# Kernel tuning notes

Measured on AMD Instinct MI355X. Metric: run time of the kernel, lower is better.

## Reference

```python
import jax, jax.numpy as jnp
import numpy as np

NUM_CLUSTERS = 64
DIM = 256
EPS = 1e-12  # torch F.normalize eps


def setup_inputs() -> dict:
    key = jax.random.key(0)
    k1, k2, k3, k4 = jax.random.split(key, 4)
    x = jax.random.normal(k1, (128, DIM, 32, 32), dtype=jnp.float32)
    # nn.Conv2d(256, K, 1) params: weight (K, C, 1, 1) -> store as (K, C); bias (K,)
    fan_in = DIM
    bound = 1.0 / np.sqrt(fan_in)
    conv_w = jax.random.uniform(k2, (NUM_CLUSTERS, DIM), jnp.float32, -bound, bound)
    conv_b = jax.random.uniform(k3, (NUM_CLUSTERS,), jnp.float32, -bound, bound)
    centroids = jax.random.uniform(k4, (NUM_CLUSTERS, DIM), jnp.float32)  # torch.rand
    return {"x": x, "conv_w": conv_w, "conv_b": conv_b, "centroids": centroids}


def _l2norm(v, axis):
    n = jnp.sqrt(jnp.sum(v * v, axis=axis, keepdims=True))
    return v / jnp.maximum(n, EPS)


def reference(x, conv_w, conv_b, centroids):
    N, C, H, W = x.shape
    K = conv_w.shape[0]
    # L2-normalize over channel dim
    x = _l2norm(x, axis=1)                      # (N, C, H, W)
    xf = x.reshape(N, C, H * W)                 # (N, C, P)
    # 1x1 conv == per-pixel linear over channels
    logits = jnp.einsum('ncp,kc->nkp', xf, conv_w) + conv_b[None, :, None]
    a = jax.nn.softmax(logits, axis=1)          # (N, K, P) softmax over clusters
    # VLAD via matmul decomposition: sum_p a[n,k,p]*(x[n,:,p] - c[k,:])
    agg = jnp.einsum('nkp,ncp->nkc', a, xf)     # (N, K, C)
    asum = jnp.sum(a, axis=-1)                  # (N, K)
    vlad = agg - asum[:, :, None] * centroids[None, :, :]
    vlad = _l2norm(vlad, axis=2)                # intra-normalization
    vlad = vlad.reshape(N, K * C)
    return _l2norm(vlad, axis=1)
```

## Files before the change

### kernel.cpp

```cpp
#include <hip/hip_runtime.h>
#include <math.h>


#define EPSF 1e-12f

typedef __attribute__((ext_vector_type(8))) __bf16 bf16x8;
typedef __attribute__((ext_vector_type(4))) float f32x4;
typedef __attribute__((ext_vector_type(4))) unsigned int u32x4;

#define MFMA(a, b, c) __builtin_amdgcn_mfma_f32_16x16x32_bf16((a), (b), (c), 0, 0, 0)

__device__ __forceinline__ bf16x8 as_bf(u32x4 v) { return __builtin_bit_cast(bf16x8, v); }

__device__ __forceinline__ unsigned packsplit(float x) {
    const unsigned u  = __float_as_uint(x);
    const unsigned hi = u & 0xFFFF0000u;
    const float lof   = x - __uint_as_float(hi);
    return hi | (__float_as_uint(lof) >> 16);
}

struct u32pair { unsigned h, l; };

__device__ __forceinline__ u32pair splitpair(float f0, float f1) {
    const unsigned u0 = __float_as_uint(f0), u1 = __float_as_uint(f1);
    u32pair r;
    r.h = __builtin_amdgcn_perm(u1, u0, 0x07060302u);
    const float l0 = f0 - __uint_as_float(u0 & 0xFFFF0000u);
    const float l1 = f1 - __uint_as_float(u1 & 0xFFFF0000u);
    r.l = __builtin_amdgcn_perm(__float_as_uint(l1), __float_as_uint(l0), 0x07060302u);
    return r;
}

__device__ __forceinline__ void unpack2q(const u32x4 q0, const u32x4 q1,
                                         u32x4& hi, u32x4& lo) {
    hi[0] = __builtin_amdgcn_perm(q0[1], q0[0], 0x07060302u);
    lo[0] = __builtin_amdgcn_perm(q0[1], q0[0], 0x05040100u);
    hi[1] = __builtin_amdgcn_perm(q0[3], q0[2], 0x07060302u);
    lo[1] = __builtin_amdgcn_perm(q0[3], q0[2], 0x05040100u);
    hi[2] = __builtin_amdgcn_perm(q1[1], q1[0], 0x07060302u);
    lo[2] = __builtin_amdgcn_perm(q1[1], q1[0], 0x05040100u);
    hi[3] = __builtin_amdgcn_perm(q1[3], q1[2], 0x07060302u);
    lo[3] = __builtin_amdgcn_perm(q1[3], q1[2], 0x05040100u);
}

__device__ __forceinline__ void split8v(const float* xv, u32x4& hi, u32x4& lo) {
    #pragma unroll
    for (int w2 = 0; w2 < 4; ++w2) {
        const u32pair r = splitpair(xv[2*w2], xv[2*w2+1]);
        hi[w2] = r.h;
        lo[w2] = r.l;
    }
}

__global__ void split_w_kernel(const float* __restrict__ wmat,
                               unsigned* __restrict__ whiG,
                               unsigned* __restrict__ wloG) {
    const int idx = blockIdx.x * 256 + threadIdx.x;
    const int mt = idx >> 9, s = (idx >> 6) & 7, l = idx & 63;
    const int k = mt * 16 + (l & 15);
    const int cb = s * 32 + 8 * (l >> 4);
    const float* wr = wmat + k * 256 + cb;
    const float4 f0 = *(const float4*)wr;
    const float4 f1 = *(const float4*)(wr + 4);
    const float xv[8] = {f0.x, f0.y, f0.z, f0.w, f1.x, f1.y, f1.z, f1.w};
    u32x4 hi, lo; split8v(xv, hi, lo);
    *(u32x4*)(whiG + idx * 4) = hi;
    *(u32x4*)(wloG + idx * 4) = lo;
}

__global__ __launch_bounds__(256, 4) void netvlad_mfma(
    const float* __restrict__ x,
    const unsigned* __restrict__ whiG, const unsigned* __restrict__ wloG,
    const float* __restrict__ bias, float* __restrict__ out,
    float* __restrict__ asum_g) {

    __shared__ __align__(16) unsigned smem[8704];
    __shared__ __align__(16) float rn_lds[128];
    unsigned* const abuf = smem;
    unsigned* const p2hi = smem;
    unsigned* const p2lo = smem + 4352;

    const int t = threadIdx.x;
    const int w = t >> 6, l = t & 63;
    const int l15 = l & 15, lg4 = l >> 4;
    const int n = blockIdx.x & 127, e = blockIdx.x >> 7;
    const size_t ximg = (size_t)n * 256 * 1024;
    const int p0 = e * 128;
    const int k0 = w * 16;
    const int cs = lg4 * 8;

    f32x4 acc1[4][2];
    #pragma unroll
    for (int i = 0; i < 4; ++i) {
        acc1[i][0] = f32x4{0.f, 0.f, 0.f, 0.f};
        acc1[i][1] = f32x4{0.f, 0.f, 0.f, 0.f};
    }
    float ssa[2] = {0.f, 0.f};

    #pragma unroll
    for (int s = 0; s < 8; ++s) {
        u32x4 wh[4], wl[4];
        #pragma unroll
        for (int mt = 0; mt < 4; ++mt) {
            const int fo = ((mt * 8 + s) * 64 + l) * 4;
            wh[mt] = *(const u32x4*)(whiG + fo);
            wl[mt] = *(const u32x4*)(wloG + fo);
        }
        #pragma unroll
        for (int ntl = 0; ntl < 2; ++ntl) {
            const float* bp = x + ximg + (size_t)(s * 32 + cs) * 1024
                              + p0 + (2 * w + ntl) * 16 + l15;
            float xv[8];
            #pragma unroll
            for (int j = 0; j < 8; ++j) xv[j] = bp[(size_t)j * 1024];
            #pragma unroll
            for (int j = 0; j < 8; ++j) ssa[ntl] = fmaf(xv[j], xv[j], ssa[ntl]);
            u32x4 bhi, blo; split8v(xv, bhi, blo);
            #pragma unroll
            for (int mt = 0; mt < 4; ++mt) {
                acc1[mt][ntl] = MFMA(as_bf(wh[mt]), as_bf(bhi), acc1[mt][ntl]);
                acc1[mt][ntl] = MFMA(as_bf(wh[mt]), as_bf(blo), acc1[mt][ntl]);
                acc1[mt][ntl] = MFMA(as_bf(wl[mt]), as_bf(bhi), acc1[mt][ntl]);
            }
        }
    }
    #pragma unroll
    for (int ntl = 0; ntl < 2; ++ntl) {
        ssa[ntl] += __shfl_xor(ssa[ntl], 16);
        ssa[ntl] += __shfl_xor(ssa[ntl], 32);
    }

    f32x4 biasv[4];
    #pragma unroll
    for (int mt = 0; mt < 4; ++mt)
        biasv[mt] = *(const f32x4*)(bias + mt * 16 + 4 * lg4);

    const int r2 = t >> 4;
    const int pq8 = (t & 15) * 8;
    const float* xg2 = x + ximg + (size_t)r2 * 1024 + p0 + pq8;
    unsigned* const w2hi = p2hi + r2 * 68 + (pq8 >> 1);
    unsigned* const w2lo = p2lo + r2 * 68 + (pq8 >> 1);
    float4 g2[4];
    #define P2_LOAD(s_) { _Pragma("unroll")                                   \
        for (int i = 0; i < 2; ++i) {                                         \
            g2[i*2]   = *(const float4*)(xg2 + (size_t)((s_)*32 + 16*i)*1024);    \
            g2[i*2+1] = *(const float4*)(xg2 + (size_t)((s_)*32 + 16*i)*1024 + 4);\
        } }
    #define P2_WRITE(b_) { _Pragma("unroll")                                  \
        for (int i = 0; i < 2; ++i) {                                         \
            u32x4 vh, vl;                                                     \
            const u32pair ra = splitpair(g2[i*2].x,   g2[i*2].y);             \
            const u32pair rb = splitpair(g2[i*2].z,   g2[i*2].w);             \
            const u32pair rc = splitpair(g2[i*2+1].x, g2[i*2+1].y);           \
            const u32pair rd = splitpair(g2[i*2+1].z, g2[i*2+1].w);           \
            vh[0] = ra.h; vl[0] = ra.l;                                       \
            vh[1] = rb.h; vl[1] = rb.l;                                       \
            vh[2] = rc.h; vl[2] = rc.l;                                       \
            vh[3] = rd.h; vl[3] = rd.l;                                       \
            *(u32x4*)(w2hi + (b_) * 2176 + i * 1088) = vh;                    \
            *(u32x4*)(w2lo + (b_) * 2176 + i * 1088) = vl; } }
    P2_LOAD(0);

    #pragma unroll
    for (int ntl = 0; ntl < 2; ++ntl) {
        const int p = (2 * w + ntl) * 16 + l15;
        const float rn = 1.f / fmaxf(sqrtf(ssa[ntl]), EPSF);
        if (lg4 == 0) rn_lds[p] = rn;
        float lgv[16];
        #pragma unroll
        for (int mt = 0; mt < 4; ++mt)
            #pragma unroll
            for (int r = 0; r < 4; ++r)
                lgv[mt * 4 + r] = fmaf(acc1[mt][ntl][r], rn, biasv[mt][r]);
        float mx = lgv[0];
        #pragma unroll
        for (int i = 1; i < 16; ++i) mx = fmaxf(mx, lgv[i]);
        mx = fmaxf(mx, __shfl_xor(mx, 16));
        mx = fmaxf(mx, __shfl_xor(mx, 32));
        float den = 0.f;
        #pragma unroll
        for (int i = 0; i < 16; ++i) { lgv[i] = __expf(lgv[i] - mx); den += lgv[i]; }
        den += __shfl_xor(den, 16);
        den += __shfl_xor(den, 32);
        const float inv = 1.f / den;
        #pragma unroll
        for (int mt = 0; mt < 4; ++mt)
            #pragma unroll
            for (int r = 0; r < 4; ++r)
                abuf[(mt * 16 + 4 * lg4 + r) * 132 + p] =
                    packsplit(lgv[mt * 4 + r] * inv);
    }
    __syncthreads();

    u32x4 aphi[4], aplo[4];
    f32x4 asum_acc = f32x4{0.f, 0.f, 0.f, 0.f};
    const u32x4 ONES = {0x3F803F80u, 0x3F803F80u, 0x3F803F80u, 0x3F803F80u};
    #pragma unroll
    for (int ks = 0; ks < 4; ++ks) {
        const unsigned* ap = abuf + (k0 + l15) * 132 + ks * 32 + cs;
        const u32x4 pa = *(const u32x4*)ap;
        const u32x4 pb = *(const u32x4*)(ap + 4);
        u32x4 ahi, alo; unpack2q(pa, pb, ahi, alo);
        asum_acc = MFMA(as_bf(ahi), as_bf(ONES), asum_acc);
        asum_acc = MFMA(as_bf(alo), as_bf(ONES), asum_acc);
        const float* rp = rn_lds + ks * 32 + cs;
        const unsigned paw[8] = {pa[0],pa[1],pa[2],pa[3],pb[0],pb[1],pb[2],pb[3]};
        float av[8];
        #pragma unroll
        for (int j = 0; j < 8; ++j) {
            const float afv = __uint_as_float(paw[j] & 0xFFFF0000u)
                            + __uint_as_float(paw[j] << 16);
            av[j] = afv * rp[j];
        }
        split8v(av, aphi[ks], aplo[ks]);
    }
    __syncthreads();

    P2_WRITE(0);

    float* op = out + (size_t)n * 16384;
    #pragma unroll
    for (int s2 = 0; s2 < 8; ++s2) {
        if (s2 < 7) P2_LOAD(s2 + 1);
        __syncthreads();
        const unsigned* shi = p2hi + (s2 & 1) * 2176;
        const unsigned* slo = p2lo + (s2 & 1) * 2176;
        f32x4 a2[2];
        #pragma unroll
        for (int ntl = 0; ntl < 2; ++ntl) {
            a2[ntl] = f32x4{0.f, 0.f, 0.f, 0.f};
            #pragma unroll
            for (int ks = 0; ks < 4; ++ks) {
                const int ro = (ntl * 16 + l15) * 68 + ks * 16 + lg4 * 4;
                const u32x4 xhi = *(const u32x4*)(shi + ro);
                const u32x4 xlo = *(const u32x4*)(slo + ro);
                a2[ntl] = MFMA(as_bf(aphi[ks]), as_bf(xhi), a2[ntl]);
                a2[ntl] = MFMA(as_bf(aphi[ks]), as_bf(xlo), a2[ntl]);
                a2[ntl] = MFMA(as_bf(aplo[ks]), as_bf(xhi), a2[ntl]);
            }
        }
        if (s2 < 7) P2_WRITE((s2 + 1) & 1);
        #pragma unroll
        for (int ntl = 0; ntl < 2; ++ntl) {
            const int c = s2 * 32 + ntl * 16 + l15;
            #pragma unroll
            for (int r = 0; r < 4; ++r)
                atomicAdd(&op[(k0 + lg4 * 4 + r) * 256 + c], a2[ntl][r]);
        }
    }
    if (l15 == 0) {
        #pragma unroll
        for (int r = 0; r < 4; ++r)
            atomicAdd(&asum_g[n * 64 + k0 + lg4 * 4 + r], asum_acc[r]);
    }
}

__global__ __launch_bounds__(256) void netvlad_epi(
    float* __restrict__ out, const float* __restrict__ asum_g,
    const float* __restrict__ cent) {
    __shared__ float wred[4];
    __shared__ float gs_sh;
    const int n = blockIdx.x;
    const int t = threadIdx.x;
    const int k = t >> 2;
    const int q = t & 3;
    float* op = out + (size_t)n * 16384 + k * 256 + q * 64;
    const float* cp = cent + k * 256 + q * 64;
    const float as = asum_g[n * 64 + k];

    float v[64];
    float ss = 0.f;
    #pragma unroll
    for (int i = 0; i < 64; i += 4) {
        const float4 av = *(const float4*)&op[i];
        const float4 cv = *(const float4*)&cp[i];
        v[i+0] = fmaf(-as, cv.x, av.x);
        v[i+1] = fmaf(-as, cv.y, av.y);
        v[i+2] = fmaf(-as, cv.z, av.z);
        v[i+3] = fmaf(-as, cv.w, av.w);
        ss = fmaf(v[i+0], v[i+0], ss);
        ss = fmaf(v[i+1], v[i+1], ss);
        ss = fmaf(v[i+2], v[i+2], ss);
        ss = fmaf(v[i+3], v[i+3], ss);
    }
    ss += __shfl_xor(ss, 1);
    ss += __shfl_xor(ss, 2);
    const float iscale = 1.f / fmaxf(sqrtf(ss), EPSF);

    float gsum = (q == 0) ? ss * iscale * iscale : 0.f;
    #pragma unroll
    for (int off = 4; off < 64; off <<= 1) gsum += __shfl_xor(gsum, off);
    if ((t & 63) == 0) wred[t >> 6] = gsum;
    __syncthreads();
    if (t == 0) {
        const float tot = wred[0] + wred[1] + wred[2] + wred[3];
        gs_sh = 1.f / fmaxf(sqrtf(tot), EPSF);
    }
    __syncthreads();
    const float fs = iscale * gs_sh;
    #pragma unroll
    for (int i = 0; i < 64; i += 4) {
        float4 w4;
        w4.x = v[i+0] * fs; w4.y = v[i+1] * fs;
        w4.z = v[i+2] * fs; w4.w = v[i+3] * fs;
        *(float4*)&op[i] = w4;
    }
}

extern "C" void kernel_launch(void* const* d_in, const int* in_sizes, int n_in,
                              void* d_out, int out_size, void* d_ws, size_t ws_size,
                              hipStream_t stream) {
    (void)in_sizes; (void)n_in; (void)ws_size;
    const float* x    = (const float*)d_in[0];
    const float* wmat = (const float*)d_in[1];
    const float* b    = (const float*)d_in[2];
    const float* cent = (const float*)d_in[3];
    float* out = (float*)d_out;
    unsigned* whiG = (unsigned*)d_ws;
    unsigned* wloG = whiG + 8192;
    float* asum_g  = (float*)(whiG + 16384);

    hipMemsetAsync(d_out, 0, (size_t)out_size * sizeof(float), stream);
    hipMemsetAsync(asum_g, 0, 128 * 64 * sizeof(float), stream);
    split_w_kernel<<<8, 256, 0, stream>>>(wmat, whiG, wloG);
    netvlad_mfma<<<1024, 256, 0, stream>>>(x, whiG, wloG, b, out, asum_g);
    netvlad_epi<<<128, 256, 0, stream>>>(out, asum_g, cent);
}
```

Before: 100.2 us.

## Split fused NetVLAD kernel into separate assignment and aggregation passes

The single kernel that computed soft assignments and then accumulated VLAD partial sums through global float atomics becomes two kernels. The first writes the normalized, packed assignment matrix to a workspace buffer and reduces asum with shuffles. The second reads x again and does the full 1024-pixel reduction per (image, channel quarter), storing results directly with no atomics or output memset. This removes heavy atomic traffic to the output, at the cost of a second full pass over x and an extra 32 MB round trip for the assignment buffer.

```diff
diff --git a/kernel.cpp b/kernel.cpp
--- a/kernel.cpp
+++ b/kernel.cpp
@@ -68,17 +68,11 @@
     *(u32x4*)(wloG + idx * 4) = lo;
 }
 
-__global__ __launch_bounds__(256, 4) void netvlad_mfma(
+__global__ __launch_bounds__(256, 4) void netvlad_p1(
     const float* __restrict__ x,
     const unsigned* __restrict__ whiG, const unsigned* __restrict__ wloG,
-    const float* __restrict__ bias, float* __restrict__ out,
+    const float* __restrict__ bias, unsigned* __restrict__ aG,
     float* __restrict__ asum_g) {
-
-    __shared__ __align__(16) unsigned smem[8704];
-    __shared__ __align__(16) float rn_lds[128];
-    unsigned* const abuf = smem;
-    unsigned* const p2hi = smem;
-    unsigned* const p2lo = smem + 4352;
 
     const int t = threadIdx.x;
     const int w = t >> 6, l = t & 63;
@@ -86,7 +80,6 @@
     const int n = blockIdx.x & 127, e = blockIdx.x >> 7;
     const size_t ximg = (size_t)n * 256 * 1024;
     const int p0 = e * 128;
-    const int k0 = w * 16;
     const int cs = lg4 * 8;
 
     f32x4 acc1[4][2];
@@ -135,37 +128,14 @@
     for (int mt = 0; mt < 4; ++mt)
         biasv[mt] = *(const f32x4*)(bias + mt * 16 + 4 * lg4);
 
-    const int r2 = t >> 4;
-    const int pq8 = (t & 15) * 8;
-    const float* xg2 = x + ximg + (size_t)r2 * 1024 + p0 + pq8;
-    unsigned* const w2hi = p2hi + r2 * 68 + (pq8 >> 1);
-    unsigned* const w2lo = p2lo + r2 * 68 + (pq8 >> 1);
-    float4 g2[4];
-    #define P2_LOAD(s_) { _Pragma("unroll")                                   \
-        for (int i = 0; i < 2; ++i) {                                         \
-            g2[i*2]   = *(const float4*)(xg2 + (size_t)((s_)*32 + 16*i)*1024);    \
-            g2[i*2+1] = *(const float4*)(xg2 + (size_t)((s_)*32 + 16*i)*1024 + 4);\
-        } }
-    #define P2_WRITE(b_) { _Pragma("unroll")                                  \
-        for (int i = 0; i < 2; ++i) {                                         \
-            u32x4 vh, vl;                                                     \
-            const u32pair ra = splitpair(g2[i*2].x,   g2[i*2].y);             \
-            const u32pair rb = splitpair(g2[i*2].z,   g2[i*2].w);             \
-            const u32pair rc = splitpair(g2[i*2+1].x, g2[i*2+1].y);           \
-            const u32pair rd = splitpair(g2[i*2+1].z, g2[i*2+1].w);           \
-            vh[0] = ra.h; vl[0] = ra.l;                                       \
-            vh[1] = rb.h; vl[1] = rb.l;                                       \
-            vh[2] = rc.h; vl[2] = rc.l;                                       \
-            vh[3] = rd.h; vl[3] = rd.l;                                       \
-            *(u32x4*)(w2hi + (b_) * 2176 + i * 1088) = vh;                    \
-            *(u32x4*)(w2lo + (b_) * 2176 + i * 1088) = vl; } }
-    P2_LOAD(0);
+    float asum_loc[16];
+    #pragma unroll
+    for (int i = 0; i < 16; ++i) asum_loc[i] = 0.f;
 
     #pragma unroll
     for (int ntl = 0; ntl < 2; ++ntl) {
-        const int p = (2 * w + ntl) * 16 + l15;
+        const int p = p0 + (2 * w + ntl) * 16 + l15;
         const float rn = 1.f / fmaxf(sqrtf(ssa[ntl]), EPSF);
-        if (lg4 == 0) rn_lds[p] = rn;
         float lgv[16];
         #pragma unroll
         for (int mt = 0; mt < 4; ++mt)
@@ -186,73 +156,70 @@
         #pragma unroll
         for (int mt = 0; mt < 4; ++mt)
             #pragma unroll
-            for (int r = 0; r < 4; ++r)
-                abuf[(mt * 16 + 4 * lg4 + r) * 132 + p] =
-                    packsplit(lgv[mt * 4 + r] * inv);
-    }
-    __syncthreads();
-
-    u32x4 aphi[4], aplo[4];
-    f32x4 asum_acc = f32x4{0.f, 0.f, 0.f, 0.f};
-    const u32x4 ONES = {0x3F803F80u, 0x3F803F80u, 0x3F803F80u, 0x3F803F80u};
-    #pragma unroll
-    for (int ks = 0; ks < 4; ++ks) {
-        const unsigned* ap = abuf + (k0 + l15) * 132 + ks * 32 + cs;
-        const u32x4 pa = *(const u32x4*)ap;
-        const u32x4 pb = *(const u32x4*)(ap + 4);
-        u32x4 ahi, alo; unpack2q(pa, pb, ahi, alo);
-        asum_acc = MFMA(as_bf(ahi), as_bf(ONES), asum_acc);
-        asum_acc = MFMA(as_bf(alo), as_bf(ONES), asum_acc);
-        const float* rp = rn_lds + ks * 32 + cs;
-        const unsigned paw[8] = {pa[0],pa[1],pa[2],pa[3],pb[0],pb[1],pb[2],pb[3]};
-        float av[8];
-        #pragma unroll
-        for (int j = 0; j < 8; ++j) {
-            const float afv = __uint_as_float(paw[j] & 0xFFFF0000u)
-                            + __uint_as_float(paw[j] << 16);
-            av[j] = afv * rp[j];
+            for (int r = 0; r < 4; ++r) {
+                const float av = lgv[mt * 4 + r] * inv;
+                asum_loc[mt * 4 + r] += av;
+                aG[((size_t)n * 64 + mt * 16 + 4 * lg4 + r) * 1024 + p] =
+                    packsplit(av * rn);
+            }
+    }
+
+    #pragma unroll
+    for (int i = 0; i < 16; ++i) {
+        float s = asum_loc[i];
+        s += __shfl_xor(s, 1);
+        s += __shfl_xor(s, 2);
+        s += __shfl_xor(s, 4);
+        s += __shfl_xor(s, 8);
+        if (l15 == 0)
+            atomicAdd(&asum_g[n * 64 + (i >> 2) * 16 + 4 * lg4 + (i & 3)], s);
+    }
+}
+
+__global__ __launch_bounds__(256, 2) void netvlad_p2(
+    const float* __restrict__ x, const unsigned* __restrict__ aG,
+    float* __restrict__ out) {
+
+    const int t = threadIdx.x;
+    const int w = t >> 6, l = t & 63;
+    const int l15 = l & 15, lg4 = l >> 4;
+    const int n = blockIdx.x >> 2, cq = blockIdx.x & 3;
+    const size_t ximg = (size_t)n * 256 * 1024;
+    const int cs = lg4 * 8;
+    const int c0 = cq * 64 + w * 16;
+
+    const float*    xrow = x  + ximg + (size_t)(c0 + l15) * 1024 + cs;
+    const unsigned* ar   = aG + ((size_t)n * 64 + l15) * 1024 + cs;
+
+    f32x4 acc[4];
+    #pragma unroll
+    for (int mt = 0; mt < 4; ++mt) acc[mt] = f32x4{0.f, 0.f, 0.f, 0.f};
+
+    #pragma unroll 4
+    for (int ks = 0; ks < 32; ++ks) {
+        float xv[8];
+        const float4 f0 = *(const float4*)(xrow + ks * 32);
+        const float4 f1 = *(const float4*)(xrow + ks * 32 + 4);
+        xv[0]=f0.x; xv[1]=f0.y; xv[2]=f0.z; xv[3]=f0.w;
+        xv[4]=f1.x; xv[5]=f1.y; xv[6]=f1.z; xv[7]=f1.w;
+        u32x4 bhi, blo; split8v(xv, bhi, blo);
+        #pragma unroll
+        for (int mt = 0; mt < 4; ++mt) {
+            const unsigned* ap = ar + (size_t)mt * 16 * 1024 + ks * 32;
+            const u32x4 pa = *(const u32x4*)ap;
+            const u32x4 pb = *(const u32x4*)(ap + 4);
+            u32x4 ahi, alo; unpack2q(pa, pb, ahi, alo);
+            acc[mt] = MFMA(as_bf(ahi), as_bf(bhi), acc[mt]);
+            acc[mt] = MFMA(as_bf(ahi), as_bf(blo), acc[mt]);
+            acc[mt] = MFMA(as_bf(alo), as_bf(bhi), acc[mt]);
         }
-        split8v(av, aphi[ks], aplo[ks]);
-    }
-    __syncthreads();
-
-    P2_WRITE(0);
-
+    }
     float* op = out + (size_t)n * 16384;
     #pragma unroll
-    for (int s2 = 0; s2 < 8; ++s2) {
-        if (s2 < 7) P2_LOAD(s2 + 1);
-        __syncthreads();
-        const unsigned* shi = p2hi + (s2 & 1) * 2176;
-        const unsigned* slo = p2lo + (s2 & 1) * 2176;
-        f32x4 a2[2];
-        #pragma unroll
-        for (int ntl = 0; ntl < 2; ++ntl) {
-            a2[ntl] = f32x4{0.f, 0.f, 0.f, 0.f};
-            #pragma unroll
-            for (int ks = 0; ks < 4; ++ks) {
-                const int ro = (ntl * 16 + l15) * 68 + ks * 16 + lg4 * 4;
-                const u32x4 xhi = *(const u32x4*)(shi + ro);
-                const u32x4 xlo = *(const u32x4*)(slo + ro);
-                a2[ntl] = MFMA(as_bf(aphi[ks]), as_bf(xhi), a2[ntl]);
-                a2[ntl] = MFMA(as_bf(aphi[ks]), as_bf(xlo), a2[ntl]);
-                a2[ntl] = MFMA(as_bf(aplo[ks]), as_bf(xhi), a2[ntl]);
-            }
-        }
-        if (s2 < 7) P2_WRITE((s2 + 1) & 1);
-        #pragma unroll
-        for (int ntl = 0; ntl < 2; ++ntl) {
-            const int c = s2 * 32 + ntl * 16 + l15;
-            #pragma unroll
-            for (int r = 0; r < 4; ++r)
-                atomicAdd(&op[(k0 + lg4 * 4 + r) * 256 + c], a2[ntl][r]);
-        }
-    }
-    if (l15 == 0) {
+    for (int mt = 0; mt < 4; ++mt)
         #pragma unroll
         for (int r = 0; r < 4; ++r)
-            atomicAdd(&asum_g[n * 64 + k0 + lg4 * 4 + r], asum_acc[r]);
-    }
+            op[(mt * 16 + 4 * lg4 + r) * 256 + c0 + l15] = acc[mt][r];
 }
 
 __global__ __launch_bounds__(256) void netvlad_epi(
@@ -310,7 +277,7 @@
 extern "C" void kernel_launch(void* const* d_in, const int* in_sizes, int n_in,
                               void* d_out, int out_size, void* d_ws, size_t ws_size,
                               hipStream_t stream) {
-    (void)in_sizes; (void)n_in; (void)ws_size;
+    (void)in_sizes; (void)n_in; (void)out_size; (void)ws_size;
     const float* x    = (const float*)d_in[0];
     const float* wmat = (const float*)d_in[1];
     const float* b    = (const float*)d_in[2];
@@ -319,10 +286,11 @@
     unsigned* whiG = (unsigned*)d_ws;
     unsigned* wloG = whiG + 8192;
     float* asum_g  = (float*)(whiG + 16384);
-
-    hipMemsetAsync(d_out, 0, (size_t)out_size * sizeof(float), stream);
+    unsigned* aG   = whiG + 24576;
+
     hipMemsetAsync(asum_g, 0, 128 * 64 * sizeof(float), stream);
     split_w_kernel<<<8, 256, 0, stream>>>(wmat, whiG, wloG);
-    netvlad_mfma<<<1024, 256, 0, stream>>>(x, whiG, wloG, b, out, asum_g);
+    netvlad_p1<<<1024, 256, 0, stream>>>(x, whiG, wloG, b, aG, asum_g);
+    netvlad_p2<<<512, 256, 0, stream>>>(x, aG, out);
     netvlad_epi<<<128, 256, 0, stream>>>(out, asum_g, cent);
 }
```

New measurement: 126.9 us. 26.7% more time.
